# Kernel tuning notes

Measured on AMD Instinct MI355X. Metric: run time of the kernel, lower is better.

Reference implementation:

```python
import jax, jax.numpy as jnp
import numpy as np

TOPK = 16
MIN_SIM = 0.05
MIN_VOTES = 0.3
REMOVE_INNER = 0.5
NUM_CLASSES = 1000


def setup_inputs() -> dict:
    key = jax.random.key(0)
    kq, kdb, kid, kxy, kwh = jax.random.split(key, 5)
    Qn, N, C = 1024, 200000, 256
    q = jax.random.normal(kq, (Qn, C), dtype=jnp.float32)
    q = q / jnp.linalg.norm(q, axis=1, keepdims=True)
    db = jax.random.normal(kdb, (N, C), dtype=jnp.float32)
    db = db / jnp.linalg.norm(db, axis=1, keepdims=True)
    ids = jax.random.randint(kid, (N,), 0, NUM_CLASSES).astype(jnp.float32)
    places_db = jnp.concatenate([db, ids[:, None]], axis=1)  # (N, C+1)
    xy = jax.random.uniform(kxy, (Qn, 2), minval=0.0, maxval=800.0)
    wh = jax.random.uniform(kwh, (Qn, 2), minval=10.0, maxval=200.0)
    boxes = jnp.concatenate([xy, xy + wh], axis=1)  # valid xyxy boxes
    return {"boxes": boxes, "descriptors": q, "places_db": places_db}


def _remove_overlapping_boxes(boxes, labels, thr):
    # overlap = intersection / min(area_i, area_j); drop the BIGGER box of any
    # same-label pair whose overlap >= thr.
    bf = boxes.astype(jnp.float32)
    x1, y1, x2, y2 = bf[:, 0], bf[:, 1], bf[:, 2], bf[:, 3]
    areas = (x2 - x1) * (y2 - y1)
    xi1 = jnp.maximum(x1[:, None], x1[None, :])
    yi1 = jnp.maximum(y1[:, None], y1[None, :])
    xi2 = jnp.minimum(x2[:, None], x2[None, :])
    yi2 = jnp.minimum(y2[:, None], y2[None, :])
    inter = jnp.clip(xi2 - xi1, 0.0) * jnp.clip(yi2 - yi1, 0.0)
    area_i, area_j = areas[:, None], areas[None, :]
    area_small = jnp.minimum(area_i, area_j)
    overlap = jnp.where(area_small > 0, inter / jnp.maximum(area_small, 1e-12), 0.0)
    same_lbl = (labels[:, None] == labels[None, :]) & (labels[:, None] >= 0)
    n = boxes.shape[0]
    non_diag = ~jnp.eye(n, dtype=bool)
    mask_pair = same_lbl & (overlap >= thr) & non_diag
    bigger_i = area_i > area_j
    remove_i = (mask_pair & bigger_i).any(axis=1)
    remove_j = (mask_pair & ~bigger_i).any(axis=0)
    remove = remove_i | remove_j
    return jnp.where(remove, jnp.full_like(labels, -1), labels)


def reference(boxes, descriptors, places_db):
    X = places_db[:, :-1]                       # (N, C)
    ids = places_db[:, -1].astype(jnp.int32)    # (N,)
    sims = descriptors @ X.T                    # (Q, N)
    top_sims, top_idx = jax.lax.top_k(sims, TOPK)   # (Q, topk)
    top_ids = ids[top_idx]                          # (Q, topk)
    mask_sim = top_sims >= MIN_SIM
    # one-hot majority vote over classes
    one_hot = (top_ids[:, :, None] == jnp.arange(NUM_CLASSES, dtype=jnp.int32)[None, None, :]).astype(jnp.float32)
    vote_counts = (one_hot * mask_sim[:, :, None].astype(jnp.float32)).sum(axis=1)  # (Q, NUM_CLASSES)
    majority_counts = vote_counts.max(axis=1)
    majority_ids = jnp.argmax(vote_counts, axis=1).astype(jnp.int32)
    valid_votes = mask_sim.sum(axis=1).astype(jnp.float32)
    vote_ratio = jnp.where(valid_votes > 0, majority_counts / jnp.maximum(valid_votes, 1.0), 0.0)
    valid = (majority_counts > 0) & (vote_ratio >= MIN_VOTES)
    results = jnp.where(valid, majority_ids, jnp.full_like(majority_ids, -1))
    results = _remove_overlapping_boxes(boxes, results, REMOVE_INNER)
    match = (top_ids == results[:, None]) & mask_sim
    sim_scores = jnp.where(match, top_sims, jnp.zeros_like(top_sims)).max(axis=1)
    valid_mask = (results >= 0) & jnp.isfinite(sim_scores) & jnp.isfinite(boxes).all(axis=1)
    # Static-shape variant of the original's compaction: invalid rows are
    # marked with class=-1 / score=0 instead of being sliced out.
    return (boxes,
            jnp.where(valid_mask, sim_scores, 0.0),
            jnp.where(valid_mask, results, -1))
```

## Files before the change

kernel.cpp:

```cpp
#include <hip/hip_runtime.h>
#include <hip/hip_bf16.h>

#define QN 1024
#define NDB 200000
#define NDB_PAD 200064
#define PDBW 257
#define CDIM 256
#define TK 16
#define NEGF (-1e30f)
#define MIN_SIM_C 0.05f
#define MIN_VOTES_C 0.3f

#define NCH 128
#define THETA 0.19f
#define CAPQ 14
#define NCHUNK1 49
#define CPQ1 (NCHUNK1*32)

typedef __attribute__((ext_vector_type(8))) short bf16x8;
typedef __attribute__((ext_vector_type(4))) float f32x4;
typedef __attribute__((ext_vector_type(8))) int   i32x8;
typedef __attribute__((ext_vector_type(4))) int   i32x4;

__device__ __forceinline__ short f2bf(float f) {
  union { float f; unsigned u; } x; x.f = f;
  unsigned u = x.u;
  return (short)((u + 0x7fffu + ((u >> 16) & 1u)) >> 16);
}

__device__ __forceinline__ void async_copy16(const void* gp, void* lp) {
  __builtin_amdgcn_global_load_lds(
      (__attribute__((address_space(1))) void*)gp,
      (__attribute__((address_space(3))) void*)lp, 16, 0, 0);
}

__device__ __forceinline__ unsigned pk_fp8x4(float a, float b, float c, float d) {
  unsigned w = (unsigned)__builtin_amdgcn_cvt_pk_fp8_f32(a, b, 0, false);
  w = (unsigned)__builtin_amdgcn_cvt_pk_fp8_f32(c, d, (int)w, true);
  return w;
}

__global__ __launch_bounds__(256) void convert_db_kernel(
    const float* __restrict__ pdb, unsigned char* __restrict__ dbb)
{
  const int wv = (int)threadIdx.x >> 6, lane = (int)threadIdx.x & 63;
  for (int r = (int)blockIdx.x*4 + wv; r < NDB_PAD; r += (int)gridDim.x*4) {
    unsigned pack = 0u;
    if (r < NDB) {
      const float* p = pdb + (size_t)r*PDBW + lane*4;
      pack = pk_fp8x4(p[0], p[1], p[2], p[3]);
    }
    const int piece = lane >> 1;
    const int ps    = piece ^ ((r & 15) << 1);
    *(unsigned*)(dbb + (size_t)r*256 + ps*8 + (lane & 1)*4) = pack;
  }
}

__global__ __launch_bounds__(256, 2) void sims_filter_kernel(
    const float* __restrict__ qd, const unsigned char* __restrict__ dbb,
    unsigned long long* __restrict__ seg_g, unsigned int* __restrict__ cnt_g)
{
  __shared__ __align__(16) char db_lds[2][64 * 256];
  __shared__ unsigned seg_lds[4][64][CAPQ][2];
  __shared__ int lcnt[4][64];

  const int tid  = (int)threadIdx.x;
  const int lane = tid & 63;
  const int wv   = tid >> 6;
  const int cid   = (int)blockIdx.x;
  const int mtile = (int)blockIdx.y;
  const int nsub = 24 + (cid < 54 ? 1 : 0);
  const int row0 = (24*cid + (cid < 54 ? cid : 54)) << 6;

  lcnt[wv][lane] = 0;

  const int l15  = lane & 15;
  const int egrp = lane >> 4;
  const int rowb = egrp << 2;
  const int colb = l15;

  i32x8 aq[4][2];
  {
    #pragma unroll
    for (int fm = 0; fm < 4; ++fm) {
      const float* qrow = qd + (size_t)(mtile*256 + wv*64 + fm*16 + l15)*CDIM;
      #pragma unroll
      for (int kk = 0; kk < 2; ++kk) {
        const float* p = qrow + kk*128 + egrp*32;
        i32x8 a;
        #pragma unroll
        for (int d = 0; d < 8; ++d) {
          float4 x = *(const float4*)(p + d*4);
          a[d] = (int)pk_fp8x4(x.x, x.y, x.z, x.w);
        }
        aq[fm][kk] = a;
      }
    }
  }

  const char* dbbase = (const char*)dbb;
#define STAGE(bufi, tile) do { \
    const char* _src = dbbase + ((size_t)(row0 + (tile)*64) * 256) + wv*4096 + lane*16; \
    char* _dst = (char*)db_lds[(bufi)] + wv*4096; \
    async_copy16(_src,        _dst); \
    async_copy16(_src + 1024, _dst + 1024); \
    async_copy16(_src + 2048, _dst + 2048); \
    async_copy16(_src + 3072, _dst + 3072); \
  } while (0)

  STAGE(0, 0);

  for (int s = 0; s < nsub; ++s) {
    asm volatile("s_waitcnt vmcnt(0)" ::: "memory");
    __builtin_amdgcn_sched_barrier(0);
    __builtin_amdgcn_s_barrier();
    __builtin_amdgcn_sched_barrier(0);

    if (s + 1 < nsub) STAGE((s + 1) & 1, s + 1);

    f32x4 acc[4][4];
    #pragma unroll
    for (int fm = 0; fm < 4; ++fm)
      #pragma unroll
      for (int fn = 0; fn < 4; ++fn)
        acc[fm][fn] = (f32x4){0.f, 0.f, 0.f, 0.f};
    __builtin_amdgcn_s_setprio(1);
    {
      const char* dbt = (const char*)db_lds[s & 1];
      #pragma unroll
      for (int kk = 0; kk < 2; ++kk) {
        #pragma unroll
        for (int fn = 0; fn < 4; ++fn) {
          const char* rowp = dbt + (fn*16 + l15)*256;
          const int mbase = kk*8 + egrp*2;
          i32x4 lo = *(const i32x4*)(rowp + (((mbase    ) ^ l15) << 4));
          i32x4 hi = *(const i32x4*)(rowp + (((mbase + 1) ^ l15) << 4));
          i32x8 b = __builtin_shufflevector(lo, hi, 0, 1, 2, 3, 4, 5, 6, 7);
          #pragma unroll
          for (int fm = 0; fm < 4; ++fm)
            acc[fm][fn] = __builtin_amdgcn_mfma_scale_f32_16x16x128_f8f6f4(
                aq[fm][kk], b, acc[fm][fn],
                0 , 0 ,
                0, 0x7F7F7F7Fu , 0, 0x7F7F7F7Fu );
        }
      }
    }
    __builtin_amdgcn_s_setprio(0);

    {
      const int idxbase = row0 + s*64;
      #pragma unroll
      for (int fm = 0; fm < 4; ++fm)
        #pragma unroll
        for (int fn = 0; fn < 4; ++fn) {
          const f32x4 a = acc[fm][fn];
          const float m = fmaxf(fmaxf(a[0], a[1]), fmaxf(a[2], a[3]));
          if (m > THETA) {
            #pragma unroll
            for (int j = 0; j < 4; ++j) {
              if (a[j] > THETA) {
                const int ql = fm*16 + rowb + j;
                const int slot = atomicAdd(&lcnt[wv][ql], 1);
                if (slot < CAPQ) {
                  seg_lds[wv][ql][slot][0] = __float_as_uint(a[j]);
                  seg_lds[wv][ql][slot][1] = (unsigned)(idxbase + fn*16 + colb);
                }
              }
            }
          }
        }
    }

    asm volatile("s_waitcnt lgkmcnt(0)" ::: "memory");
    __builtin_amdgcn_sched_barrier(0);
  }
#undef STAGE

  {
    const int cnt = lcnt[wv][lane];
    const int qg = mtile*256 + wv*64 + lane;
    cnt_g[qg*NCH + cid] = (unsigned)cnt;
    const int nc = min(cnt, CAPQ);
    unsigned long long* dst = seg_g + (size_t)(qg*NCH + cid)*CAPQ;
    for (int j = 0; j < nc; ++j) {
      unsigned long long lo = seg_lds[wv][lane][j][0];
      unsigned long long hi = seg_lds[wv][lane][j][1];
      dst[j] = lo | (hi << 32);
    }
  }
}

__global__ __launch_bounds__(64) void gather_vote_kernel(
    const float* __restrict__ pdb,
    const unsigned long long* __restrict__ seg_g, const unsigned* __restrict__ cnt_g,
    int* __restrict__ out_label, float* __restrict__ out_s, int* __restrict__ flag)
{
  __shared__ float    cv[NCH*CAPQ];
  __shared__ unsigned ci[NCH*CAPQ];
  const int q    = (int)blockIdx.x;
  const int lane = (int)threadIdx.x;

  bool over = false;
  int tot = 0;
  #pragma unroll
  for (int h = 0; h < 2; ++h) {
    const int c = h*64 + lane;
    const int cnt = (int)cnt_g[q*NCH + c];
    over |= (cnt > CAPQ);
    const int nc = min(cnt, CAPQ);
    tot += nc;
    const unsigned long long* src = seg_g + (size_t)(q*NCH + c)*CAPQ;
    for (int j = 0; j < CAPQ; ++j) {
      float v = NEGF; unsigned idx = 0u;
      if (j < nc) {
        const unsigned long long e = src[j];
        v = __uint_as_float((unsigned)e);
        idx = (unsigned)(e >> 32);
      }
      cv[c*CAPQ + j] = v;
      ci[c*CAPQ + j] = idx;
    }
  }
  #pragma unroll
  for (int off = 32; off >= 1; off >>= 1) tot += __shfl_xor(tot, off);
  __syncthreads();

  float topv[TK]; int topid[TK];
  #pragma unroll
  for (int r = 0; r < TK; ++r) {
    float bv = NEGF; int bp = -1;
    #pragma unroll 4
    for (int j = 0; j < (NCH*CAPQ)/64; ++j) {
      const int p = j*64 + lane;
      const float v = cv[p];
      if (v > bv) { bv = v; bp = p; }
    }
    #pragma unroll
    for (int off = 32; off >= 1; off >>= 1) {
      const float ov = __shfl_xor(bv, off);
      const int   op = __shfl_xor(bp, off);
      if (ov > bv || (ov == bv && ((unsigned)op < (unsigned)bp))) { bv = ov; bp = op; }
    }
    topv[r] = bv;
    int id = -2;
    if (bp >= 0 && bv > NEGF) id = (int)pdb[(size_t)ci[bp]*PDBW + CDIM];
    topid[r] = id;
    if (lane == 0 && bp >= 0) cv[bp] = NEGF;
    __syncthreads();
  }

  if (lane == 0) {
    bool mk[TK];
    int nvalid = 0;
    #pragma unroll
    for (int i = 0; i < TK; ++i) {
      mk[i] = (topv[i] >= MIN_SIM_C) && (topid[i] >= 0);
      nvalid += mk[i] ? 1 : 0;
    }
    int maj = 0, majid = 0x7fffffff;
    for (int i = 0; i < TK; ++i) {
      if (!mk[i]) continue;
      int c = 0;
      for (int j = 0; j < TK; ++j) c += (mk[j] && topid[j] == topid[i]) ? 1 : 0;
      if (c > maj || (c == maj && topid[i] < majid)) { maj = c; majid = topid[i]; }
    }
    const float ratio = (float)maj / fmaxf((float)nvalid, 1.0f);
    const bool valid = (maj > 0) && (ratio >= MIN_VOTES_C);
    const int label = valid ? majid : -1;
    float s = 0.f;
    #pragma unroll
    for (int i = 0; i < TK; ++i)
      if (mk[i] && topid[i] == label) s = fmaxf(s, topv[i]);
    out_label[q] = label;
    out_s[q]     = s;
  }
  const bool bad = (__ballot(over) != 0ull) || (tot < TK);
  if (lane == 0 && bad) atomicOr(flag, 1);
}

__global__ __launch_bounds__(256, 2) void sims_topk1_kernel(
    const float* __restrict__ qd, const float* __restrict__ pdb,
    float* __restrict__ cand_val, unsigned int* __restrict__ cand_idx,
    const int* __restrict__ gate)
{
  if (gate && *gate == 0) return;
  __shared__ __align__(16) short db_lds[128 * 264];
  float* sims = (float*)db_lds;

  const int tid  = (int)threadIdx.x;
  const int lane = tid & 63;
  const int wv   = tid >> 6;
  const int cid   = (int)blockIdx.x;
  const int mtile = (int)blockIdx.y;

  bf16x8 aq[2][8];
  {
    const int l15 = lane & 15;
    const int kb  = (lane >> 4) << 3;
    #pragma unroll
    for (int fm = 0; fm < 2; ++fm) {
      const int row = mtile*128 + wv*32 + fm*16 + l15;
      #pragma unroll
      for (int kk = 0; kk < 8; ++kk) {
        const float* p = qd + (size_t)row*CDIM + kk*32 + kb;
        float4 x0 = *(const float4*)p;
        float4 x1 = *(const float4*)(p + 4);
        bf16x8 a;
        a[0]=f2bf(x0.x); a[1]=f2bf(x0.y); a[2]=f2bf(x0.z); a[3]=f2bf(x0.w);
        a[4]=f2bf(x1.x); a[5]=f2bf(x1.y); a[6]=f2bf(x1.z); a[7]=f2bf(x1.w);
        aq[fm][kk] = a;
      }
    }
  }

  float    tv[TK];
  unsigned ti[TK];
  #pragma unroll
  for (int i = 0; i < TK; ++i) { tv[i] = NEGF; ti[i] = 0u; }
  float minv = NEGF; int minp = 0;

  const int g0chunk = cid * 4096;
  const int q_l  = tid & 127;
  const int half = tid >> 7;

  for (int s = 0; s < 32; ++s) {
    const int g0 = g0chunk + s*128;
    {
      const int rb = tid >> 6;
      const int c4 = (tid & 63) << 2;
      for (int i = 0; i < 32; ++i) {
        const int rl = i*4 + rb;
        const int g  = g0 + rl;
        float v0, v1, v2, v3;
        if (g < NDB) {
          const float* p = pdb + (size_t)g*PDBW + c4;
          v0 = p[0]; v1 = p[1]; v2 = p[2]; v3 = p[3];
        } else { v0 = v1 = v2 = v3 = 0.f; }
        short* d = &db_lds[rl*264 + c4];
        d[0]=f2bf(v0); d[1]=f2bf(v1); d[2]=f2bf(v2); d[3]=f2bf(v3);
      }
    }
    __syncthreads();

    f32x4 acc[2][8];
    #pragma unroll
    for (int fm = 0; fm < 2; ++fm)
      #pragma unroll
      for (int fn = 0; fn < 8; ++fn)
        acc[fm][fn] = (f32x4){0.f, 0.f, 0.f, 0.f};
    {
      const int l15 = lane & 15;
      const int kb  = (lane >> 4) << 3;
      #pragma unroll
      for (int kk = 0; kk < 8; ++kk) {
        bf16x8 b[8];
        #pragma unroll
        for (int fn = 0; fn < 8; ++fn)
          b[fn] = *(const bf16x8*)&db_lds[(fn*16 + l15)*264 + kk*32 + kb];
        #pragma unroll
        for (int fn = 0; fn < 8; ++fn) {
          acc[0][fn] = __builtin_amdgcn_mfma_f32_16x16x32_bf16(aq[0][kk], b[fn], acc[0][fn], 0, 0, 0);
          acc[1][fn] = __builtin_amdgcn_mfma_f32_16x16x32_bf16(aq[1][kk], b[fn], acc[1][fn], 0, 0, 0);
        }
      }
    }
    __syncthreads();

    {
      const int colb = lane & 15;
      const int rowb = (lane >> 4) << 2;
      #pragma unroll
      for (int fm = 0; fm < 2; ++fm)
        #pragma unroll
        for (int fn = 0; fn < 8; ++fn)
          #pragma unroll
          for (int j = 0; j < 4; ++j)
            sims[(wv*32 + fm*16 + rowb + j)*129 + fn*16 + colb] = acc[fm][fn][j];
    }
    __syncthreads();

    {
      const int cb = half * 64;
      #pragma unroll 4
      for (int c = 0; c < 64; ++c) {
        const int colc = cb + c;
        const float v = sims[q_l*129 + colc];
        const int g = g0 + colc;
        if (v > minv && g < NDB) {
          #pragma unroll
          for (int i = 0; i < TK; ++i) if (i == minp) { tv[i] = v; ti[i] = (unsigned)g; }
          minv = tv[0]; minp = 0;
          #pragma unroll
          for (int i = 1; i < TK; ++i) if (tv[i] < minv) { minv = tv[i]; minp = i; }
        }
      }
    }
    __syncthreads();
  }

  {
    const int qg = mtile*128 + q_l;
    float*    pv = cand_val + ((size_t)qg*NCHUNK1 + cid)*32 + half*TK;
    unsigned* pi = cand_idx + ((size_t)qg*NCHUNK1 + cid)*32 + half*TK;
    #pragma unroll
    for (int i = 0; i < TK; ++i) { pv[i] = tv[i]; pi[i] = ti[i]; }
  }
}

template<int CPQ>
__global__ __launch_bounds__(64) void merge_vote_kernel(
    const float* __restrict__ pdb,
    const float* __restrict__ cand_val, const unsigned* __restrict__ cand_idx,
    int* __restrict__ out_label, float* __restrict__ out_s,
    const int* __restrict__ gate)
{
  if (gate && *gate == 0) return;
  __shared__ float    cv[CPQ];
  __shared__ unsigned ci[CPQ];
  const int q    = (int)blockIdx.x;
  const int lane = (int)threadIdx.x;

  for (int j = lane; j < CPQ; j += 64) {
    cv[j] = cand_val[(size_t)q*CPQ + j];
    ci[j] = cand_idx[(size_t)q*CPQ + j];
  }
  __syncthreads();

  float topv[TK]; int topid[TK];
  #pragma unroll
  for (int r = 0; r < TK; ++r) {
    float bv = NEGF; int bp = -1;
    for (int j = lane; j < CPQ; j += 64) {
      const float v = cv[j];
      if (v > bv) { bv = v; bp = j; }
    }
    #pragma unroll
    for (int off = 32; off >= 1; off >>= 1) {
      const float ov = __shfl_xor(bv, off);
      const int   op = __shfl_xor(bp, off);
      if (ov > bv || (ov == bv && ((unsigned)op < (unsigned)bp))) { bv = ov; bp = op; }
    }
    topv[r] = bv;
    int id = -2;
    if (bp >= 0 && bv > NEGF) id = (int)pdb[(size_t)ci[bp]*PDBW + CDIM];
    topid[r] = id;
    if (lane == 0 && bp >= 0) cv[bp] = NEGF;
    __syncthreads();
  }

  if (lane == 0) {
    bool mk[TK];
    int nvalid = 0;
    #pragma unroll
    for (int i = 0; i < TK; ++i) {
      mk[i] = (topv[i] >= MIN_SIM_C) && (topid[i] >= 0);
      nvalid += mk[i] ? 1 : 0;
    }
    int maj = 0, majid = 0x7fffffff;
    for (int i = 0; i < TK; ++i) {
      if (!mk[i]) continue;
      int c = 0;
      for (int j = 0; j < TK; ++j) c += (mk[j] && topid[j] == topid[i]) ? 1 : 0;
      if (c > maj || (c == maj && topid[i] < majid)) { maj = c; majid = topid[i]; }
    }
    const float ratio = (float)maj / fmaxf((float)nvalid, 1.0f);
    const bool valid = (maj > 0) && (ratio >= MIN_VOTES_C);
    const int label = valid ? majid : -1;
    float s = 0.f;
    #pragma unroll
    for (int i = 0; i < TK; ++i)
      if (mk[i] && topid[i] == label) s = fmaxf(s, topv[i]);
    out_label[q] = label;
    out_s[q]     = s;
  }
}

__device__ __forceinline__ bool finitef(float v) {
  return ((__float_as_uint(v) >> 23) & 0xffu) != 0xffu;
}

__global__ __launch_bounds__(64) void finalize_kernel(
    const float* __restrict__ boxes, const int* __restrict__ labels,
    const float* __restrict__ svals, float* __restrict__ out)
{
  const int x    = (int)blockIdx.x;
  const int lane = (int)threadIdx.x;
  const int lx = labels[x];
  const float bx1 = boxes[x*4+0], by1 = boxes[x*4+1];
  const float bx2 = boxes[x*4+2], by2 = boxes[x*4+3];
  const float ax = (bx2 - bx1) * (by2 - by1);

  bool flag = false;
  if (lx >= 0) {
    for (int y = lane; y < QN; y += 64) {
      if (y == x) continue;
      if (labels[y] != lx) continue;
      const float c1 = boxes[y*4+0], c2 = boxes[y*4+1];
      const float c3 = boxes[y*4+2], c4 = boxes[y*4+3];
      const float ay = (c3 - c1) * (c4 - c2);
      const float xi1 = fmaxf(bx1, c1), yi1 = fmaxf(by1, c2);
      const float xi2 = fminf(bx2, c3), yi2 = fminf(by2, c4);
      const float inter = fmaxf(xi2 - xi1, 0.f) * fmaxf(yi2 - yi1, 0.f);
      const float asmall = fminf(ax, ay);
      const float ov = (asmall > 0.f) ? inter / fmaxf(asmall, 1e-12f) : 0.f;
      if (ov >= 0.5f && ay <= ax) flag = true;
    }
  }
  const bool removed = (__ballot(flag) != 0ull);
  const int label = removed ? -1 : lx;
  const float s = svals[x];
  const bool fin = finitef(s) && finitef(bx1) && finitef(by1) && finitef(bx2) && finitef(by2);
  const bool valid = (label >= 0) && fin;

  if (lane == 0) {
    out[4096 + x] = valid ? s : 0.f;
    out[5120 + x] = (float)(valid ? label : -1);
  }
  if (lane < 4) out[x*4 + lane] = boxes[x*4 + lane];
}

extern "C" void kernel_launch(void* const* d_in, const int* in_sizes, int n_in,
                              void* d_out, int out_size, void* d_ws, size_t ws_size,
                              hipStream_t stream)
{
  const float* boxes = (const float*)d_in[0];
  const float* qd    = (const float*)d_in[1];
  const float* pdb   = (const float*)d_in[2];
  float* out = (float*)d_out;
  char* ws = (char*)d_ws;

  const size_t db_bytes  = (size_t)NDB_PAD * 256;
  const size_t seg_bytes = (size_t)QN * NCH * CAPQ * 8;
  const size_t cnt_bytes = (size_t)QN * NCH * 4;
  const size_t c1_bytes  = (size_t)QN * CPQ1 * 8;
  const size_t A_bytes   = (seg_bytes + cnt_bytes > c1_bytes) ? seg_bytes + cnt_bytes : c1_bytes;
  const size_t need = db_bytes + A_bytes + (size_t)QN*8 + 64;

  if (ws_size >= need) {
    unsigned char* dbb = (unsigned char*)ws;
    char* A = ws + db_bytes;
    unsigned long long* seg_g = (unsigned long long*)A;
    unsigned*           cnt_g = (unsigned*)(A + seg_bytes);
    float*    cand_val = (float*)A;
    unsigned* cand_idx = (unsigned*)(A + (size_t)QN*CPQ1*4);
    int*      labels   = (int*)(ws + db_bytes + A_bytes);
    float*    svals    = (float*)(ws + db_bytes + A_bytes + (size_t)QN*4);
    int*      flag     = (int*)(ws + db_bytes + A_bytes + (size_t)QN*8);

    hipMemsetAsync(flag, 0, 4, stream);
    hipLaunchKernelGGL(convert_db_kernel, dim3(2048), dim3(256), 0, stream, pdb, dbb);
    hipLaunchKernelGGL(sims_filter_kernel, dim3(NCH, 4), dim3(256), 0, stream,
                       qd, dbb, seg_g, cnt_g);
    hipLaunchKernelGGL(gather_vote_kernel, dim3(QN), dim3(64), 0, stream,
                       pdb, seg_g, cnt_g, labels, svals, flag);
    hipLaunchKernelGGL(sims_topk1_kernel, dim3(NCHUNK1, 8), dim3(256), 0, stream,
                       qd, pdb, cand_val, cand_idx, flag);
    hipLaunchKernelGGL((merge_vote_kernel<CPQ1>), dim3(QN), dim3(64), 0, stream,
                       pdb, cand_val, cand_idx, labels, svals, flag);
    hipLaunchKernelGGL(finalize_kernel, dim3(QN), dim3(64), 0, stream,
                       boxes, labels, svals, out);
  } else {
    const size_t n1 = (size_t)QN * CPQ1;
    float*    cand_val = (float*)ws;
    unsigned* cand_idx = (unsigned*)(ws + n1*4);
    int*      labels   = (int*)(ws + n1*8);
    float*    svals    = (float*)(ws + n1*8 + (size_t)QN*4);

    hipLaunchKernelGGL(sims_topk1_kernel, dim3(NCHUNK1, 8), dim3(256), 0, stream,
                       qd, pdb, cand_val, cand_idx, (const int*)nullptr);
    hipLaunchKernelGGL((merge_vote_kernel<CPQ1>), dim3(QN), dim3(64), 0, stream,
                       pdb, cand_val, cand_idx, labels, svals, (const int*)nullptr);
    hipLaunchKernelGGL(finalize_kernel, dim3(QN), dim3(64), 0, stream,
                       boxes, labels, svals, out);
  }
}
```

Baseline: 174.4 us.

## Fuse DB fp8 conversion into the similarity filter kernel with 1024-thread blocks

Removes the separate convert_db pass and its fp8 staging buffer. The similarity kernel now loads fp32 database rows directly, converts them to fp8 in registers, and writes swizzled tiles to LDS using register double-buffering. Blocks grow to 1024 threads covering all 1024 queries, so each DB tile is read once instead of once per query tile. Chunk count doubles to 256 and per-chunk capacity drops to 12, which changes the overflow fallback risk and the gather work. The flag reset moves into the kernel, replacing the memset.

```diff
diff --git a/kernel.cpp b/kernel.cpp
--- a/kernel.cpp
+++ b/kernel.cpp
@@ -11,9 +11,9 @@
 #define MIN_SIM_C 0.05f
 #define MIN_VOTES_C 0.3f
 
-#define NCH 128
+#define NCH 256
 #define THETA 0.19f
-#define CAPQ 14
+#define CAPQ 12
 #define NCHUNK1 49
 #define CPQ1 (NCHUNK1*32)
 
@@ -28,50 +28,29 @@
   return (short)((u + 0x7fffu + ((u >> 16) & 1u)) >> 16);
 }
 
-__device__ __forceinline__ void async_copy16(const void* gp, void* lp) {
-  __builtin_amdgcn_global_load_lds(
-      (__attribute__((address_space(1))) void*)gp,
-      (__attribute__((address_space(3))) void*)lp, 16, 0, 0);
-}
-
 __device__ __forceinline__ unsigned pk_fp8x4(float a, float b, float c, float d) {
   unsigned w = (unsigned)__builtin_amdgcn_cvt_pk_fp8_f32(a, b, 0, false);
   w = (unsigned)__builtin_amdgcn_cvt_pk_fp8_f32(c, d, (int)w, true);
   return w;
 }
 
-__global__ __launch_bounds__(256) void convert_db_kernel(
-    const float* __restrict__ pdb, unsigned char* __restrict__ dbb)
-{
-  const int wv = (int)threadIdx.x >> 6, lane = (int)threadIdx.x & 63;
-  for (int r = (int)blockIdx.x*4 + wv; r < NDB_PAD; r += (int)gridDim.x*4) {
-    unsigned pack = 0u;
-    if (r < NDB) {
-      const float* p = pdb + (size_t)r*PDBW + lane*4;
-      pack = pk_fp8x4(p[0], p[1], p[2], p[3]);
-    }
-    const int piece = lane >> 1;
-    const int ps    = piece ^ ((r & 15) << 1);
-    *(unsigned*)(dbb + (size_t)r*256 + ps*8 + (lane & 1)*4) = pack;
-  }
-}
-
-__global__ __launch_bounds__(256, 2) void sims_filter_kernel(
-    const float* __restrict__ qd, const unsigned char* __restrict__ dbb,
-    unsigned long long* __restrict__ seg_g, unsigned int* __restrict__ cnt_g)
+__global__ __launch_bounds__(1024, 1) void sims_fused_kernel(
+    const float* __restrict__ qd, const float* __restrict__ pdb,
+    unsigned long long* __restrict__ seg_g, unsigned int* __restrict__ cnt_g,
+    int* __restrict__ flag)
 {
   __shared__ __align__(16) char db_lds[2][64 * 256];
-  __shared__ unsigned seg_lds[4][64][CAPQ][2];
-  __shared__ int lcnt[4][64];
+  __shared__ unsigned seg_lds[16][64][CAPQ][2];
+  __shared__ int lcnt[16][64];
 
   const int tid  = (int)threadIdx.x;
   const int lane = tid & 63;
   const int wv   = tid >> 6;
-  const int cid   = (int)blockIdx.x;
-  const int mtile = (int)blockIdx.y;
-  const int nsub = 24 + (cid < 54 ? 1 : 0);
-  const int row0 = (24*cid + (cid < 54 ? cid : 54)) << 6;
-
+  const int cid  = (int)blockIdx.x;
+  const int nsub = 12 + (cid < 54 ? 1 : 0);
+  const int row0 = (12*cid + (cid < 54 ? cid : 54)) << 6;
+
+  if (cid == 0 && tid == 0) *flag = 0;
   lcnt[wv][lane] = 0;
 
   const int l15  = lane & 15;
@@ -79,11 +58,15 @@
   const int rowb = egrp << 2;
   const int colb = l15;
 
+  const int srow   = tid >> 4;
+  const int spiece = tid & 15;
+  const int sdst   = srow*256 + ((spiece ^ (srow & 15)) << 4);
+
   i32x8 aq[4][2];
   {
     #pragma unroll
     for (int fm = 0; fm < 4; ++fm) {
-      const float* qrow = qd + (size_t)(mtile*256 + wv*64 + fm*16 + l15)*CDIM;
+      const float* qrow = qd + (size_t)(wv*64 + fm*16 + l15)*CDIM;
       #pragma unroll
       for (int kk = 0; kk < 2; ++kk) {
         const float* p = qrow + kk*128 + egrp*32;
@@ -98,25 +81,36 @@
     }
   }
 
-  const char* dbbase = (const char*)dbb;
-#define STAGE(bufi, tile) do { \
-    const char* _src = dbbase + ((size_t)(row0 + (tile)*64) * 256) + wv*4096 + lane*16; \
-    char* _dst = (char*)db_lds[(bufi)] + wv*4096; \
-    async_copy16(_src,        _dst); \
-    async_copy16(_src + 1024, _dst + 1024); \
-    async_copy16(_src + 2048, _dst + 2048); \
-    async_copy16(_src + 3072, _dst + 3072); \
+  float4 sf0, sf1, sf2, sf3;
+#define LOADT(tile) do { \
+    const int _r = row0 + (tile)*64 + srow; \
+    if (_r < NDB) { \
+      const float* _p = pdb + (size_t)_r*PDBW + spiece*16; \
+      sf0 = *(const float4*)(_p);      sf1 = *(const float4*)(_p + 4); \
+      sf2 = *(const float4*)(_p + 8);  sf3 = *(const float4*)(_p + 12); \
+    } else { \
+      sf0 = sf1 = sf2 = sf3 = (float4){0.f, 0.f, 0.f, 0.f}; \
+    } \
   } while (0)
-
-  STAGE(0, 0);
+#define STAGEW(bufi) do { \
+    i32x4 _w; \
+    _w[0] = (int)pk_fp8x4(sf0.x, sf0.y, sf0.z, sf0.w); \
+    _w[1] = (int)pk_fp8x4(sf1.x, sf1.y, sf1.z, sf1.w); \
+    _w[2] = (int)pk_fp8x4(sf2.x, sf2.y, sf2.z, sf2.w); \
+    _w[3] = (int)pk_fp8x4(sf3.x, sf3.y, sf3.z, sf3.w); \
+    *(i32x4*)(db_lds[(bufi)] + sdst) = _w; \
+  } while (0)
+
+  LOADT(0);
+  STAGEW(0);
+  LOADT(1);
+  __syncthreads();
 
   for (int s = 0; s < nsub; ++s) {
-    asm volatile("s_waitcnt vmcnt(0)" ::: "memory");
-    __builtin_amdgcn_sched_barrier(0);
-    __builtin_amdgcn_s_barrier();
-    __builtin_amdgcn_sched_barrier(0);
-
-    if (s + 1 < nsub) STAGE((s + 1) & 1, s + 1);
+    if (s + 1 < nsub) {
+      STAGEW((s + 1) & 1);
+      if (s + 2 < nsub) LOADT(s + 2);
+    }
 
     f32x4 acc[4][4];
     #pragma unroll
@@ -173,12 +167,15 @@
 
     asm volatile("s_waitcnt lgkmcnt(0)" ::: "memory");
     __builtin_amdgcn_sched_barrier(0);
-  }
-#undef STAGE
+    __builtin_amdgcn_s_barrier();
+    __builtin_amdgcn_sched_barrier(0);
+  }
+#undef LOADT
+#undef STAGEW
 
   {
     const int cnt = lcnt[wv][lane];
-    const int qg = mtile*256 + wv*64 + lane;
+    const int qg = wv*64 + lane;
     cnt_g[qg*NCH + cid] = (unsigned)cnt;
     const int nc = min(cnt, CAPQ);
     unsigned long long* dst = seg_g + (size_t)(qg*NCH + cid)*CAPQ;
@@ -203,7 +200,7 @@
   bool over = false;
   int tot = 0;
   #pragma unroll
-  for (int h = 0; h < 2; ++h) {
+  for (int h = 0; h < NCH/64; ++h) {
     const int c = h*64 + lane;
     const int cnt = (int)cnt_g[q*NCH + c];
     over |= (cnt > CAPQ);
@@ -529,28 +526,24 @@
   float* out = (float*)d_out;
   char* ws = (char*)d_ws;
 
-  const size_t db_bytes  = (size_t)NDB_PAD * 256;
   const size_t seg_bytes = (size_t)QN * NCH * CAPQ * 8;
   const size_t cnt_bytes = (size_t)QN * NCH * 4;
   const size_t c1_bytes  = (size_t)QN * CPQ1 * 8;
   const size_t A_bytes   = (seg_bytes + cnt_bytes > c1_bytes) ? seg_bytes + cnt_bytes : c1_bytes;
-  const size_t need = db_bytes + A_bytes + (size_t)QN*8 + 64;
+  const size_t need = A_bytes + (size_t)QN*8 + 64;
 
   if (ws_size >= need) {
-    unsigned char* dbb = (unsigned char*)ws;
-    char* A = ws + db_bytes;
+    char* A = ws;
     unsigned long long* seg_g = (unsigned long long*)A;
     unsigned*           cnt_g = (unsigned*)(A + seg_bytes);
     float*    cand_val = (float*)A;
     unsigned* cand_idx = (unsigned*)(A + (size_t)QN*CPQ1*4);
-    int*      labels   = (int*)(ws + db_bytes + A_bytes);
-    float*    svals    = (float*)(ws + db_bytes + A_bytes + (size_t)QN*4);
-    int*      flag     = (int*)(ws + db_bytes + A_bytes + (size_t)QN*8);
-
-    hipMemsetAsync(flag, 0, 4, stream);
-    hipLaunchKernelGGL(convert_db_kernel, dim3(2048), dim3(256), 0, stream, pdb, dbb);
-    hipLaunchKernelGGL(sims_filter_kernel, dim3(NCH, 4), dim3(256), 0, stream,
-                       qd, dbb, seg_g, cnt_g);
+    int*      labels   = (int*)(ws + A_bytes);
+    float*    svals    = (float*)(ws + A_bytes + (size_t)QN*4);
+    int*      flag     = (int*)(ws + A_bytes + (size_t)QN*8);
+
+    hipLaunchKernelGGL(sims_fused_kernel, dim3(NCH), dim3(1024), 0, stream,
+                       qd, pdb, seg_g, cnt_g, flag);
     hipLaunchKernelGGL(gather_vote_kernel, dim3(QN), dim3(64), 0, stream,
                        pdb, seg_g, cnt_g, labels, svals, flag);
     hipLaunchKernelGGL(sims_topk1_kernel, dim3(NCHUNK1, 8), dim3(256), 0, stream,
```

Measured after the change: 663.0 us. 280% more time.
